# Optimization experiments

Hardware: AMD Instinct MI355X
Metric: run time of the kernel (lower is better)

Reference implementation:

```python
import jax, jax.numpy as jnp
import numpy as np

ALPHA = 0.2  # LeakyReLU negative slope (module init arg)


def setup_inputs() -> dict:
    key = jax.random.key(0)
    ks = jax.random.split(key, 5)
    b, w, K, E = 8, 256, 256, 512  # batch, window_size, n_features, embed (=2*window)
    x = jax.random.normal(ks[0], (b, w, K), dtype=jnp.float32)
    W = jax.random.normal(ks[1], (E, 2 * w), dtype=jnp.float32) * 0.05
    b_lin = jax.random.normal(ks[2], (E,), dtype=jnp.float32) * 0.05
    a = jax.random.normal(ks[3], (E,), dtype=jnp.float32) * 0.05
    bias = jax.random.normal(ks[4], (K, K), dtype=jnp.float32) * 0.05
    return {"x": x, "W": W, "b_lin": b_lin, "a": a, "bias": bias}


def reference(x, W, b_lin, a, bias):
    # x: (b, window, K) -> v: (b, K, window)
    v = jnp.transpose(x, (0, 2, 1))
    w = v.shape[2]
    # lin(concat(v_i, v_j)) == v_i @ Wl^T + v_j @ Wr^T + b_lin  (split weight)
    Wl, Wr = W[:, :w], W[:, w:]
    left = jnp.einsum('bkw,ew->bke', v, Wl)    # (b, K, E)
    right = jnp.einsum('bkw,ew->bke', v, Wr)   # (b, K, E)
    pre = left[:, :, None, :] + right[:, None, :, :] + b_lin  # (b, K, K, E)
    act = jax.nn.leaky_relu(pre, negative_slope=ALPHA)
    e = jnp.einsum('bije,e->bij', act, a) + bias               # (b, K, K)
    attn = jax.nn.softmax(e, axis=2)  # dropout p=0 in eval -> identity
    h = jax.nn.sigmoid(jnp.einsum('bij,bjw->biw', attn, v))    # (b, K, window)
    return jnp.transpose(h, (0, 2, 1))                          # (b, window, K)
```

## Files before the change

kernel.cpp:

```cpp
#include <hip/hip_runtime.h>
#include <math.h>

typedef float f32x4 __attribute__((ext_vector_type(4)));
typedef __bf16 bf16x8 __attribute__((ext_vector_type(8)));
typedef unsigned short u16x8 __attribute__((ext_vector_type(8)));

__device__ __forceinline__ unsigned short f2bf(float f) {
    union { float f; unsigned int u; } v; v.f = f;
    unsigned int u = v.u;
    return (unsigned short)((u + 0x7fffu + ((u >> 16) & 1u)) >> 16);
}
__device__ __forceinline__ float bf_lo(unsigned int d) {
    union { unsigned int u; float f; } v; v.u = d << 16; return v.f;
}
__device__ __forceinline__ float bf_hi(unsigned int d) {
    union { unsigned int u; float f; } v; v.u = d & 0xffff0000u; return v.f;
}
__device__ __forceinline__ float sigmoidf_(float v) {
    return 1.f / (1.f + __expf(-v));
}

__global__ __launch_bounds__(256) void mfma_gemm_kernel(
    const float* __restrict__ x,
    const float* __restrict__ W,
    const float* __restrict__ b_lin,
    float* __restrict__ Lp,
    unsigned short* __restrict__ R2)
{
    const int b = blockIdx.y;
    const int t = blockIdx.x;
    const bool left = (t < 32);
    int m0, n0;
    if (left) { m0 = (t >> 3) * 64; n0 = (t & 7) * 64; }
    else      { const int tt = t - 32; m0 = (tt >> 2) * 64; n0 = (tt & 3) * 64; }

    __shared__ unsigned short As[64][72];
    __shared__ unsigned short Bs[64][72];

    unsigned short (*Ts)[72] = left ? As : Bs;
    unsigned short (*Ds)[72] = left ? Bs : As;
    const int cbase = left ? m0 : n0;
    const int rbase = left ? n0 : m0;
    const int coff  = left ? 0 : 256;

    const int tid  = threadIdx.x;
    const int wv   = tid >> 6;
    const int lane = tid & 63;
    const int wy = wv >> 1, wx = wv & 1;
    const int lr = lane & 15;
    const int lk = lane >> 4;

    const float* xb = x + b * 65536;

    f32x4 acc[2][2];
    #pragma unroll
    for (int i = 0; i < 2; i++)
        #pragma unroll
        for (int jj = 0; jj < 2; jj++) acc[i][jj] = (f32x4){0.f, 0.f, 0.f, 0.f};

    const int wl = tid >> 4;
    const int kg = tid & 15;
    const int dr = tid >> 2;
    const int dc = (tid & 3) * 16;

    for (int k0 = 0; k0 < 256; k0 += 64) {
        #pragma unroll
        for (int p = 0; p < 4; p++) {
            const int w = wl + 16 * p;
            const float4 v = *(const float4*)(xb + (k0 + w) * 256 + cbase + kg * 4);
            Ts[kg * 4 + 0][w] = f2bf(v.x);
            Ts[kg * 4 + 1][w] = f2bf(v.y);
            Ts[kg * 4 + 2][w] = f2bf(v.z);
            Ts[kg * 4 + 3][w] = f2bf(v.w);
        }
        {
            const float* src = W + (rbase + dr) * 512 + coff + k0 + dc;
            const float4 v0 = *(const float4*)(src);
            const float4 v1 = *(const float4*)(src + 4);
            const float4 v2 = *(const float4*)(src + 8);
            const float4 v3 = *(const float4*)(src + 12);
            u16x8 o0, o1;
            o0[0] = f2bf(v0.x); o0[1] = f2bf(v0.y); o0[2] = f2bf(v0.z); o0[3] = f2bf(v0.w);
            o0[4] = f2bf(v1.x); o0[5] = f2bf(v1.y); o0[6] = f2bf(v1.z); o0[7] = f2bf(v1.w);
            o1[0] = f2bf(v2.x); o1[1] = f2bf(v2.y); o1[2] = f2bf(v2.z); o1[3] = f2bf(v2.w);
            o1[4] = f2bf(v3.x); o1[5] = f2bf(v3.y); o1[6] = f2bf(v3.z); o1[7] = f2bf(v3.w);
            *(u16x8*)&Ds[dr][dc]     = o0;
            *(u16x8*)&Ds[dr][dc + 8] = o1;
        }
        __syncthreads();
        #pragma unroll
        for (int kk = 0; kk < 64; kk += 32) {
            const bf16x8 a0 = *(const bf16x8*)&As[wy * 32 + lr][kk + lk * 8];
            const bf16x8 a1 = *(const bf16x8*)&As[wy * 32 + 16 + lr][kk + lk * 8];
            const bf16x8 b0 = *(const bf16x8*)&Bs[wx * 32 + lr][kk + lk * 8];
            const bf16x8 b1 = *(const bf16x8*)&Bs[wx * 32 + 16 + lr][kk + lk * 8];
            acc[0][0] = __builtin_amdgcn_mfma_f32_16x16x32_bf16(a0, b0, acc[0][0], 0, 0, 0);
            acc[0][1] = __builtin_amdgcn_mfma_f32_16x16x32_bf16(a0, b1, acc[0][1], 0, 0, 0);
            acc[1][0] = __builtin_amdgcn_mfma_f32_16x16x32_bf16(a1, b0, acc[1][0], 0, 0, 0);
            acc[1][1] = __builtin_amdgcn_mfma_f32_16x16x32_bf16(a1, b1, acc[1][1], 0, 0, 0);
        }
        __syncthreads();
    }

    if (left) {
        #pragma unroll
        for (int mi = 0; mi < 2; mi++) {
            #pragma unroll
            for (int ni = 0; ni < 2; ni++) {
                const int row = m0 + wy * 32 + mi * 16 + lk * 4;
                const int col = n0 + wx * 32 + ni * 16 + lr;
                const float bl = b_lin[col];
                #pragma unroll
                for (int r = 0; r < 4; r++)
                    Lp[b * 131072 + (row + r) * 512 + col] = acc[mi][ni][r] + bl;
            }
        }
    } else {
        unsigned short* R2b = R2 + b * 131072;
        #pragma unroll
        for (int mi = 0; mi < 2; mi++) {
            #pragma unroll
            for (int ni = 0; ni < 2; ni++) {
                const int row = m0 + wy * 32 + mi * 16 + lk * 4;
                const int col = n0 + wx * 32 + ni * 16 + lr;
                ushort4 o;
                o.x = f2bf(acc[mi][ni][0]);
                o.y = f2bf(acc[mi][ni][1]);
                o.z = f2bf(acc[mi][ni][2]);
                o.w = f2bf(acc[mi][ni][3]);
                *(ushort4*)(R2b + (row >> 3) * 2048 + col * 8 + (row & 7)) = o;
            }
        }
    }
}

__global__ __launch_bounds__(512, 8) void attn_kernel(
    const float* __restrict__ x,
    const float* __restrict__ Lp,
    const unsigned int* __restrict__ R2u,
    const float* __restrict__ a,
    const float* __restrict__ bias,
    float* __restrict__ out)
{
    const int b   = blockIdx.x & 7;
    const int i0  = (blockIdx.x >> 3) * 4;
    const int tid = threadIdx.x;
    const int j   = tid & 255;
    const int eh  = tid >> 8;

    __shared__ float Lt[512][4];
    __shared__ float aS[512];
    __shared__ float acc2P[2][4][256];
    __shared__ float rgp[2][256];
    __shared__ float u15s[4];
    __shared__ unsigned short atbf[16 * 264];

    {
        const int i  = tid >> 7;
        const int e0 = (tid & 127) * 4;
        const float4 v = *(const float4*)(Lp + b * 131072 + (i0 + i) * 512 + e0);
        Lt[e0 + 0][i] = v.x;
        Lt[e0 + 1][i] = v.y;
        Lt[e0 + 2][i] = v.z;
        Lt[e0 + 3][i] = v.w;
        aS[tid] = a[tid];
    }

    if (tid < 256) {
        const int i = tid >> 6, lane = tid & 63;
        const float* Lr = Lp + b * 131072 + (i0 + i) * 512 + lane * 8;
        const float* ar = a + lane * 8;
        const float4 la = *(const float4*)Lr;
        const float4 lb = *(const float4*)(Lr + 4);
        const float4 ca = *(const float4*)ar;
        const float4 cb = *(const float4*)(ar + 4);
        float p = la.x * ca.x + la.y * ca.y + la.z * ca.z + la.w * ca.w
                + lb.x * cb.x + lb.y * cb.y + lb.z * cb.z + lb.w * cb.w;
        #pragma unroll
        for (int off = 32; off; off >>= 1) p += __shfl_xor(p, off);
        if (lane == 0) u15s[i] = 0.6f * p;
    }
    __syncthreads();

    const float* aq = aS + eh * 256;
    const float (*Ltq)[4] = (const float (*)[4])(Lt + eh * 256);
    const uint4* Rq = (const uint4*)(R2u + b * 65536) + (eh * 32) * 256 + j;

    float acc0 = 0.f, acc1 = 0.f, acc2 = 0.f, acc3 = 0.f, rsum = 0.f;

    uint4 cur = Rq[0];
    for (int tk = 0; tk < 32; tk++) {
        uint4 nxt;
        if (tk < 31) nxt = Rq[(tk + 1) * 256];
        float r[8];
        r[0] = bf_lo(cur.x); r[1] = bf_hi(cur.x);
        r[2] = bf_lo(cur.y); r[3] = bf_hi(cur.y);
        r[4] = bf_lo(cur.z); r[5] = bf_hi(cur.z);
        r[6] = bf_lo(cur.w); r[7] = bf_hi(cur.w);
        #pragma unroll
        for (int q2 = 0; q2 < 2; q2++) {
            const float4 av4 = *(const float4*)&aq[tk * 8 + q2 * 4];
            #pragma unroll
            for (int s = 0; s < 4; s++) {
                const int e = tk * 8 + q2 * 4 + s;
                const float4 lv = *(const float4*)Ltq[e];
                const float ae = ((const float*)&av4)[s];
                const float rv = r[q2 * 4 + s];
                rsum = fmaf(ae, rv, rsum);
                acc0 = fmaf(ae, fabsf(lv.x + rv), acc0);
                acc1 = fmaf(ae, fabsf(lv.y + rv), acc1);
                acc2 = fmaf(ae, fabsf(lv.z + rv), acc2);
                acc3 = fmaf(ae, fabsf(lv.w + rv), acc3);
            }
        }
        cur = nxt;
    }
    acc2P[eh][0][j] = acc0;
    acc2P[eh][1][j] = acc1;
    acc2P[eh][2][j] = acc2;
    acc2P[eh][3][j] = acc3;
    rgp[eh][j] = rsum;
    __syncthreads();

    if (tid < 256) {
        const int i = tid >> 6, lane = tid & 63;
        const float u15 = u15s[i];
        float v[4];
        float m = -1e30f;
        #pragma unroll
        for (int u = 0; u < 4; u++) {
            const int jj = lane + 64 * u;
            const float uR = rgp[0][jj] + rgp[1][jj];
            const float ab = acc2P[0][i][jj] + acc2P[1][i][jj];
            v[u] = u15 + 0.6f * uR + 0.4f * ab + bias[(i0 + i) * 256 + jj];
            m = fmaxf(m, v[u]);
        }
        #pragma unroll
        for (int off = 32; off; off >>= 1) m = fmaxf(m, __shfl_xor(m, off));
        float s = 0.f;
        #pragma unroll
        for (int u = 0; u < 4; u++) { v[u] = __expf(v[u] - m); s += v[u]; }
        #pragma unroll
        for (int off = 32; off; off >>= 1) s += __shfl_xor(s, off);
        const float inv = 1.f / s;
        #pragma unroll
        for (int u = 0; u < 4; u++)
            atbf[i * 264 + lane + 64 * u] = f2bf(v[u] * inv);
    }
    __syncthreads();

    {
        const int wvv  = tid >> 6;
        const int lane = tid & 63;
        const int lr = lane & 15;
        const int lk = lane >> 4;
        #pragma unroll
        for (int half = 0; half < 2; half++) {
            const int nt = wvv + half * 8;
            f32x4 hacc = (f32x4){0.f, 0.f, 0.f, 0.f};
            const float* xw = x + b * 65536 + (nt * 16 + lr) * 256;
            #pragma unroll
            for (int kt = 0; kt < 8; kt++) {
                const bf16x8 av = *(const bf16x8*)&atbf[lr * 264 + kt * 32 + lk * 8];
                const float4 f0 = *(const float4*)(xw + kt * 32 + lk * 8);
                const float4 f1 = *(const float4*)(xw + kt * 32 + lk * 8 + 4);
                u16x8 bu;
                bu[0] = f2bf(f0.x); bu[1] = f2bf(f0.y); bu[2] = f2bf(f0.z); bu[3] = f2bf(f0.w);
                bu[4] = f2bf(f1.x); bu[5] = f2bf(f1.y); bu[6] = f2bf(f1.z); bu[7] = f2bf(f1.w);
                const bf16x8 bv = *(const bf16x8*)&bu;
                hacc = __builtin_amdgcn_mfma_f32_16x16x32_bf16(av, bv, hacc, 0, 0, 0);
            }
            if (lk == 0) {
                float4 o;
                o.x = sigmoidf_(hacc[0]);
                o.y = sigmoidf_(hacc[1]);
                o.z = sigmoidf_(hacc[2]);
                o.w = sigmoidf_(hacc[3]);
                *(float4*)(out + b * 65536 + (nt * 16 + lr) * 256 + i0) = o;
            }
        }
    }
}

extern "C" void kernel_launch(void* const* d_in, const int* in_sizes, int n_in,
                              void* d_out, int out_size, void* d_ws, size_t ws_size,
                              hipStream_t stream) {
    const float* x     = (const float*)d_in[0];
    const float* W     = (const float*)d_in[1];
    const float* b_lin = (const float*)d_in[2];
    const float* a     = (const float*)d_in[3];
    const float* bias  = (const float*)d_in[4];
    float* out = (float*)d_out;

    char* ws = (char*)d_ws;
    float*          Lp = (float*)ws;
    unsigned short* R2 = (unsigned short*)(ws + (4 << 20));

    mfma_gemm_kernel<<<dim3(64, 8), 256, 0, stream>>>(x, W, b_lin, Lp, R2);
    attn_kernel<<<512, 512, 0, stream>>>(x, Lp, (const unsigned int*)R2, a, bias, out);
}
```

Before: 108.0 us.

## Pre-convert x to bf16, interleave L layout, and widen attention blocks to 1024 threads

```diff
diff --git a/kernel.cpp b/kernel.cpp
--- a/kernel.cpp
+++ b/kernel.cpp
@@ -24,11 +24,24 @@
     const float* __restrict__ x,
     const float* __restrict__ W,
     const float* __restrict__ b_lin,
-    float* __restrict__ Lp,
-    unsigned short* __restrict__ R2)
+    float* __restrict__ LpT,
+    unsigned short* __restrict__ R2,
+    unsigned short* __restrict__ xbf)
 {
     const int b = blockIdx.y;
     const int t = blockIdx.x;
+
+    if (t >= 64) {
+        const int idx = b * 65536 + (t - 64) * 2048 + threadIdx.x * 8;
+        const float4 v0 = *(const float4*)(x + idx);
+        const float4 v1 = *(const float4*)(x + idx + 4);
+        u16x8 o;
+        o[0] = f2bf(v0.x); o[1] = f2bf(v0.y); o[2] = f2bf(v0.z); o[3] = f2bf(v0.w);
+        o[4] = f2bf(v1.x); o[5] = f2bf(v1.y); o[6] = f2bf(v1.z); o[7] = f2bf(v1.w);
+        *(u16x8*)(xbf + idx) = o;
+        return;
+    }
+
     const bool left = (t < 32);
     int m0, n0;
     if (left) { m0 = (t >> 3) * 64; n0 = (t & 7) * 64; }
@@ -110,9 +123,12 @@
                 const int row = m0 + wy * 32 + mi * 16 + lk * 4;
                 const int col = n0 + wx * 32 + ni * 16 + lr;
                 const float bl = b_lin[col];
-                #pragma unroll
-                for (int r = 0; r < 4; r++)
-                    Lp[b * 131072 + (row + r) * 512 + col] = acc[mi][ni][r] + bl;
+                float4 o;
+                o.x = acc[mi][ni][0] + bl;
+                o.y = acc[mi][ni][1] + bl;
+                o.z = acc[mi][ni][2] + bl;
+                o.w = acc[mi][ni][3] + bl;
+                *(float4*)(LpT + b * 131072 + (row >> 2) * 2048 + col * 4) = o;
             }
         }
     } else {
@@ -134,64 +150,65 @@
     }
 }
 
-__global__ __launch_bounds__(512, 8) void attn_kernel(
-    const float* __restrict__ x,
-    const float* __restrict__ Lp,
+__global__ __launch_bounds__(1024, 8) void attn_kernel(
+    const unsigned short* __restrict__ xbf,
+    const float* __restrict__ LpT,
     const unsigned int* __restrict__ R2u,
     const float* __restrict__ a,
     const float* __restrict__ bias,
     float* __restrict__ out)
 {
-    const int b   = blockIdx.x & 7;
-    const int i0  = (blockIdx.x >> 3) * 4;
-    const int tid = threadIdx.x;
-    const int j   = tid & 255;
-    const int eh  = tid >> 8;
-
-    __shared__ float Lt[512][4];
-    __shared__ float aS[512];
-    __shared__ float acc2P[2][4][256];
-    __shared__ float rgp[2][256];
+    const int b     = blockIdx.x & 7;
+    const int itile = blockIdx.x >> 3;
+    const int i0    = itile * 4;
+    const int tid   = threadIdx.x;
+    const int j     = tid & 255;
+    const int wv    = tid >> 6;
+    const int lane  = tid & 63;
+
+    __shared__ float acc2P[4][4][256];
+    __shared__ float rgp[4][256];
+    __shared__ float u15p[8][4];
     __shared__ float u15s[4];
     __shared__ unsigned short atbf[16 * 264];
 
-    {
-        const int i  = tid >> 7;
-        const int e0 = (tid & 127) * 4;
-        const float4 v = *(const float4*)(Lp + b * 131072 + (i0 + i) * 512 + e0);
-        Lt[e0 + 0][i] = v.x;
-        Lt[e0 + 1][i] = v.y;
-        Lt[e0 + 2][i] = v.z;
-        Lt[e0 + 3][i] = v.w;
-        aS[tid] = a[tid];
-    }
-
-    if (tid < 256) {
-        const int i = tid >> 6, lane = tid & 63;
-        const float* Lr = Lp + b * 131072 + (i0 + i) * 512 + lane * 8;
-        const float* ar = a + lane * 8;
-        const float4 la = *(const float4*)Lr;
-        const float4 lb = *(const float4*)(Lr + 4);
-        const float4 ca = *(const float4*)ar;
-        const float4 cb = *(const float4*)(ar + 4);
-        float p = la.x * ca.x + la.y * ca.y + la.z * ca.z + la.w * ca.w
-                + lb.x * cb.x + lb.y * cb.y + lb.z * cb.z + lb.w * cb.w;
-        #pragma unroll
-        for (int off = 32; off; off >>= 1) p += __shfl_xor(p, off);
-        if (lane == 0) u15s[i] = 0.6f * p;
+    const int ehq = __builtin_amdgcn_readfirstlane(tid >> 8);
+
+    if (tid < 512) {
+        const float4 lv = *(const float4*)(LpT + b * 131072 + itile * 2048 + tid * 4);
+        const float ae = a[tid];
+        float p0 = ae * lv.x, p1 = ae * lv.y, p2 = ae * lv.z, p3 = ae * lv.w;
+        #pragma unroll
+        for (int off = 32; off; off >>= 1) {
+            p0 += __shfl_xor(p0, off);
+            p1 += __shfl_xor(p1, off);
+            p2 += __shfl_xor(p2, off);
+            p3 += __shfl_xor(p3, off);
+        }
+        if (lane == 0) {
+            u15p[wv][0] = p0; u15p[wv][1] = p1;
+            u15p[wv][2] = p2; u15p[wv][3] = p3;
+        }
     }
     __syncthreads();
-
-    const float* aq = aS + eh * 256;
-    const float (*Ltq)[4] = (const float (*)[4])(Lt + eh * 256);
-    const uint4* Rq = (const uint4*)(R2u + b * 65536) + (eh * 32) * 256 + j;
+    if (tid < 4) {
+        float s = 0.f;
+        #pragma unroll
+        for (int q = 0; q < 8; q++) s += u15p[q][tid];
+        u15s[tid] = 0.6f * s;
+    }
+
+    const float* Lq = LpT + b * 131072 + itile * 2048 + ehq * 512;
+    const float* aq = a + ehq * 128;
+    const uint4* Rq = (const uint4*)(R2u + b * 65536) + (ehq * 16) * 256 + j;
 
     float acc0 = 0.f, acc1 = 0.f, acc2 = 0.f, acc3 = 0.f, rsum = 0.f;
 
     uint4 cur = Rq[0];
-    for (int tk = 0; tk < 32; tk++) {
+    #pragma unroll 2
+    for (int tk = 0; tk < 16; tk++) {
         uint4 nxt;
-        if (tk < 31) nxt = Rq[(tk + 1) * 256];
+        if (tk < 15) nxt = Rq[(tk + 1) * 256];
         float r[8];
         r[0] = bf_lo(cur.x); r[1] = bf_hi(cur.x);
         r[2] = bf_lo(cur.y); r[3] = bf_hi(cur.y);
@@ -199,11 +216,11 @@
         r[6] = bf_lo(cur.w); r[7] = bf_hi(cur.w);
         #pragma unroll
         for (int q2 = 0; q2 < 2; q2++) {
-            const float4 av4 = *(const float4*)&aq[tk * 8 + q2 * 4];
+            const float4 av4 = *(const float4*)(aq + tk * 8 + q2 * 4);
             #pragma unroll
             for (int s = 0; s < 4; s++) {
                 const int e = tk * 8 + q2 * 4 + s;
-                const float4 lv = *(const float4*)Ltq[e];
+                const float4 lv = *(const float4*)(Lq + e * 4);
                 const float ae = ((const float*)&av4)[s];
                 const float rv = r[q2 * 4 + s];
                 rsum = fmaf(ae, rv, rsum);
@@ -215,34 +232,35 @@
         }
         cur = nxt;
     }
-    acc2P[eh][0][j] = acc0;
-    acc2P[eh][1][j] = acc1;
-    acc2P[eh][2][j] = acc2;
-    acc2P[eh][3][j] = acc3;
-    rgp[eh][j] = rsum;
+    acc2P[ehq][0][j] = acc0;
+    acc2P[ehq][1][j] = acc1;
+    acc2P[ehq][2][j] = acc2;
+    acc2P[ehq][3][j] = acc3;
+    rgp[ehq][j] = rsum;
     __syncthreads();
 
-    if (tid < 256) {
-        const int i = tid >> 6, lane = tid & 63;
+    if (wv < 4) {
+        const int i = wv;
         const float u15 = u15s[i];
         float v[4];
         float m = -1e30f;
         #pragma unroll
         for (int u = 0; u < 4; u++) {
             const int jj = lane + 64 * u;
-            const float uR = rgp[0][jj] + rgp[1][jj];
-            const float ab = acc2P[0][i][jj] + acc2P[1][i][jj];
+            const float uR = rgp[0][jj] + rgp[1][jj] + rgp[2][jj] + rgp[3][jj];
+            const float ab = acc2P[0][i][jj] + acc2P[1][i][jj]
+                           + acc2P[2][i][jj] + acc2P[3][i][jj];
             v[u] = u15 + 0.6f * uR + 0.4f * ab + bias[(i0 + i) * 256 + jj];
             m = fmaxf(m, v[u]);
         }
         #pragma unroll
         for (int off = 32; off; off >>= 1) m = fmaxf(m, __shfl_xor(m, off));
-        float s = 0.f;
-        #pragma unroll
-        for (int u = 0; u < 4; u++) { v[u] = __expf(v[u] - m); s += v[u]; }
-        #pragma unroll
-        for (int off = 32; off; off >>= 1) s += __shfl_xor(s, off);
-        const float inv = 1.f / s;
+        float ssum = 0.f;
+        #pragma unroll
+        for (int u = 0; u < 4; u++) { v[u] = __expf(v[u] - m); ssum += v[u]; }
+        #pragma unroll
+        for (int off = 32; off; off >>= 1) ssum += __shfl_xor(ssum, off);
+        const float inv = 1.f / ssum;
         #pragma unroll
         for (int u = 0; u < 4; u++)
             atbf[i * 264 + lane + 64 * u] = f2bf(v[u] * inv);
@@ -250,34 +268,23 @@
     __syncthreads();
 
     {
-        const int wvv  = tid >> 6;
-        const int lane = tid & 63;
         const int lr = lane & 15;
         const int lk = lane >> 4;
-        #pragma unroll
-        for (int half = 0; half < 2; half++) {
-            const int nt = wvv + half * 8;
-            f32x4 hacc = (f32x4){0.f, 0.f, 0.f, 0.f};
-            const float* xw = x + b * 65536 + (nt * 16 + lr) * 256;
-            #pragma unroll
-            for (int kt = 0; kt < 8; kt++) {
-                const bf16x8 av = *(const bf16x8*)&atbf[lr * 264 + kt * 32 + lk * 8];
-                const float4 f0 = *(const float4*)(xw + kt * 32 + lk * 8);
-                const float4 f1 = *(const float4*)(xw + kt * 32 + lk * 8 + 4);
-                u16x8 bu;
-                bu[0] = f2bf(f0.x); bu[1] = f2bf(f0.y); bu[2] = f2bf(f0.z); bu[3] = f2bf(f0.w);
-                bu[4] = f2bf(f1.x); bu[5] = f2bf(f1.y); bu[6] = f2bf(f1.z); bu[7] = f2bf(f1.w);
-                const bf16x8 bv = *(const bf16x8*)&bu;
-                hacc = __builtin_amdgcn_mfma_f32_16x16x32_bf16(av, bv, hacc, 0, 0, 0);
-            }
-            if (lk == 0) {
-                float4 o;
-                o.x = sigmoidf_(hacc[0]);
-                o.y = sigmoidf_(hacc[1]);
-                o.z = sigmoidf_(hacc[2]);
-                o.w = sigmoidf_(hacc[3]);
-                *(float4*)(out + b * 65536 + (nt * 16 + lr) * 256 + i0) = o;
-            }
+        f32x4 hacc = (f32x4){0.f, 0.f, 0.f, 0.f};
+        const unsigned short* xw = xbf + b * 65536 + (wv * 16 + lr) * 256;
+        #pragma unroll
+        for (int kt = 0; kt < 8; kt++) {
+            const bf16x8 av = *(const bf16x8*)&atbf[lr * 264 + kt * 32 + lk * 8];
+            const bf16x8 bv = *(const bf16x8*)(xw + kt * 32 + lk * 8);
+            hacc = __builtin_amdgcn_mfma_f32_16x16x32_bf16(av, bv, hacc, 0, 0, 0);
+        }
+        if (lk == 0) {
+            float4 o;
+            o.x = sigmoidf_(hacc[0]);
+            o.y = sigmoidf_(hacc[1]);
+            o.z = sigmoidf_(hacc[2]);
+            o.w = sigmoidf_(hacc[3]);
+            *(float4*)(out + b * 65536 + (wv * 16 + lr) * 256 + i0) = o;
         }
     }
 }
@@ -293,9 +300,10 @@
     float* out = (float*)d_out;
 
     char* ws = (char*)d_ws;
-    float*          Lp = (float*)ws;
-    unsigned short* R2 = (unsigned short*)(ws + (4 << 20));
-
-    mfma_gemm_kernel<<<dim3(64, 8), 256, 0, stream>>>(x, W, b_lin, Lp, R2);
-    attn_kernel<<<512, 512, 0, stream>>>(x, Lp, (const unsigned int*)R2, a, bias, out);
-}
+    float*          LpT = (float*)ws;
+    unsigned short* R2  = (unsigned short*)(ws + (4 << 20));
+    unsigned short* xbf = (unsigned short*)(ws + (6 << 20));
+
+    mfma_gemm_kernel<<<dim3(96, 8), 256, 0, stream>>>(x, W, b_lin, LpT, R2, xbf);
+    attn_kernel<<<512, 1024, 0, stream>>>(xbf, LpT, (const unsigned int*)R2, a, bias, out);
+}
```

After: 101.2 us. 1.07x faster.
